# Kernel optimization log

Measured on AMD Instinct MI355X. Metric: run time of the kernel, lower is better.

## Reference

```python
import jax, jax.numpy as jnp
import numpy as np

B, N, DIN, DOUT = 8, 2048, 512, 512
EDGE_P = 0.01  # edge probability for the random binary adjacency


def setup_inputs() -> dict:
    key = jax.random.key(0)
    k1, k2, k3, k4 = jax.random.split(key, 4)
    inputs = jax.random.normal(k1, (B, N, DIN), dtype=jnp.float32)
    # binary dense adjacency (dense_to_sparse discards weights -> edges are adj != 0)
    adj = (jax.random.uniform(k2, (B, N, N)) < EDGE_P).astype(jnp.float32)
    W = jax.random.normal(k3, (DIN, DOUT), dtype=jnp.float32) / np.sqrt(DIN)
    b = jax.random.normal(k4, (DOUT,), dtype=jnp.float32) * 0.01
    return {"inputs": inputs, "adj": adj, "W": W, "b": b}


def _gcn_norm(adj):
    # binary edge mask (edge weights from dense_to_sparse are discarded)
    A = (adj != 0).astype(adj.dtype)
    # add remaining self-loops: force diagonal to 1
    eye = jnp.eye(A.shape[-1], dtype=A.dtype)
    A = jnp.maximum(A, eye)
    deg = A.sum(axis=-1)                       # [B, N]
    dinv = jnp.where(deg > 0, jax.lax.rsqrt(deg), 0.0)
    # D^-1/2 (A + I) D^-1/2
    return dinv[..., :, None] * A * dinv[..., None, :]


def reference(inputs, adj, W, b):
    norm = _gcn_norm(adj)                      # [B, N, N]
    h = jnp.einsum('bnf,fo->bno', inputs, W)   # linear (no internal bias)
    agg = jnp.einsum('bnm,bmo->bno', norm, h)  # degree-normalized aggregation
    return jnp.tanh(agg + b)
```

## Files before the change

### kernel.cpp

```cpp
#include <hip/hip_runtime.h>
#include <hip/hip_bf16.h>
#include <math.h>


#define NROWS 16384
#define NCOLS 2048
#define DF    512
#define CAP   64

typedef __attribute__((ext_vector_type(8))) short bf16x8;
typedef __attribute__((ext_vector_type(4))) float f32x4;
typedef const void __attribute__((address_space(1))) gvoid_t;
typedef void __attribute__((address_space(3))) svoid_t;

__global__ __launch_bounds__(256) void scan_wt_cvt(
    const float* __restrict__ W, __hip_bfloat16* __restrict__ WT,
    const float* __restrict__ adj, int* __restrict__ cnt,
    int* __restrict__ edges, float* __restrict__ dinv,
    const float* __restrict__ X, __hip_bfloat16* __restrict__ Xb) {
  __shared__ float t[64][65];
  const int blk = blockIdx.x;
  const int tid = threadIdx.x;
  if (blk < 64) {
    const int bx = blk & 7, by = blk >> 3;
    const int tx = tid & 63, ty = tid >> 6;
    #pragma unroll
    for (int i = 0; i < 16; ++i)
      t[ty + i * 4][tx] = W[(size_t)(by * 64 + ty + i * 4) * DF + bx * 64 + tx];
    __syncthreads();
    #pragma unroll
    for (int i = 0; i < 16; ++i)
      WT[(size_t)(bx * 64 + ty + i * 4) * DF + by * 64 + tx] =
          __float2bfloat16(t[tx][ty + i * 4]);
    return;
  }
  if (blk >= 1088) {
    const int b = blk - 1088;
    const float4* X4 = (const float4*)X;
    ushort4* O4 = (ushort4*)Xb;
    #pragma unroll
    for (int i = 0; i < 4; ++i) {
      const int idx = b * 1024 + i * 256 + tid;
      const float4 v = X4[idx];
      union { ushort4 u; __hip_bfloat16 h[4]; } p;
      p.h[0] = __float2bfloat16(v.x);
      p.h[1] = __float2bfloat16(v.y);
      p.h[2] = __float2bfloat16(v.z);
      p.h[3] = __float2bfloat16(v.w);
      O4[idx] = p.u;
    }
    return;
  }
  const int lane = tid & 63;
  const int wv = tid >> 6;
  const int rbase = (blk - 64) * 16 + wv * 4;
  float4 cur[8], nxt[8];
  {
    const float4* r4 = (const float4*)(adj + (size_t)rbase * NCOLS);
    #pragma unroll
    for (int k = 0; k < 8; ++k) cur[k] = r4[k * 64 + lane];
  }
  #pragma unroll
  for (int g = 0; g < 4; ++g) {
    const int r = rbase + g;
    if (g < 3) {
      const float4* rn = (const float4*)(adj + (size_t)(r + 1) * NCOLS);
      #pragma unroll
      for (int k = 0; k < 8; ++k) nxt[k] = rn[k * 64 + lane];
    }
    const int n = r & (NCOLS - 1);
    unsigned m = 0;
    #pragma unroll
    for (int k = 0; k < 8; ++k) {
      m |= (cur[k].x != 0.0f ? 1u : 0u) << (4 * k);
      m |= (cur[k].y != 0.0f ? 1u : 0u) << (4 * k + 1);
      m |= (cur[k].z != 0.0f ? 1u : 0u) << (4 * k + 2);
      m |= (cur[k].w != 0.0f ? 1u : 0u) << (4 * k + 3);
    }
    if (lane == ((n >> 2) & 63))
      m |= 1u << (((n >> 8) << 2) | (n & 3));
    const int c_ = __popc(m);
    int inc = c_;
    #pragma unroll
    for (int off = 1; off < 64; off <<= 1) {
      const int tv = __shfl_up(inc, off);
      if (lane >= off) inc += tv;
    }
    const int tot = __shfl(inc, 63);
    int p = inc - c_;
    unsigned mm = m;
    const size_t eb = (size_t)r * CAP;
    while (mm) {
      const int bpos = __ffs(mm) - 1;
      mm &= mm - 1;
      if (p < CAP)
        edges[eb + p] = ((bpos >> 2) << 8) + (lane << 2) + (bpos & 3);
      ++p;
    }
    if (lane == 63) {
      cnt[r] = tot < CAP ? tot : CAP;
      dinv[r] = rsqrtf((float)tot);
    }
    #pragma unroll
    for (int k = 0; k < 8; ++k) cur[k] = nxt[k];
  }
}

__global__ __launch_bounds__(256) void gemm_k(
    const __hip_bfloat16* __restrict__ A, const __hip_bfloat16* __restrict__ BT,
    __hip_bfloat16* __restrict__ H) {
  __shared__ __hip_bfloat16 As[2][128 * 32];
  __shared__ __hip_bfloat16 Bs[2][128 * 32];
  const int tid = threadIdx.x;
  const int lane = tid & 63;
  const int w = tid >> 6;
  const int id = blockIdx.x;
  const int xcd = id & 7;
  const int jj = id >> 3;
  const int bm = (xcd * 16 + (jj >> 2)) * 128;
  const int bn = (jj & 3) * 128;

  const int wm = (w >> 1) * 64;
  const int wn = (w & 1) * 64;
  const int srow = tid >> 2;
  const int scol = (tid & 3) * 8;
  const int kl = (lane >> 4) * 8;
  const int rl = lane & 15;

  f32x4 acc[4][4] = {};

  #define STAGE(k0, buf)  do {                                          \
    _Pragma("unroll")                                                   \
    for (int i = 0; i < 2; ++i) {                                       \
      const __hip_bfloat16* ga = A  + (size_t)(bm + i * 64 + srow) * DF + (k0) + scol; \
      const __hip_bfloat16* gb = BT + (size_t)(bn + i * 64 + srow) * DF + (k0) + scol; \
      char* la = (char*)&As[buf][0] + i * 4096 + w * 1024;              \
      char* lb = (char*)&Bs[buf][0] + i * 4096 + w * 1024;              \
      __builtin_amdgcn_global_load_lds((gvoid_t*)ga, (svoid_t*)la, 16, 0, 0); \
      __builtin_amdgcn_global_load_lds((gvoid_t*)gb, (svoid_t*)lb, 16, 0, 0); \
    } } while (0)

  STAGE(0, 0);
  __syncthreads();

  for (int tIt = 0; tIt < 16; ++tIt) {
    const int c_ = tIt & 1, nx = c_ ^ 1;
    if (tIt < 15) STAGE((tIt + 1) * 32, nx);
    bf16x8 af[4], bf[4];
    #pragma unroll
    for (int mi = 0; mi < 4; ++mi)
      af[mi] = *(const bf16x8*)&As[c_][(wm + mi * 16 + rl) * 32 + kl];
    #pragma unroll
    for (int ni = 0; ni < 4; ++ni)
      bf[ni] = *(const bf16x8*)&Bs[c_][(wn + ni * 16 + rl) * 32 + kl];
    #pragma unroll
    for (int mi = 0; mi < 4; ++mi)
      #pragma unroll
      for (int ni = 0; ni < 4; ++ni)
        acc[mi][ni] = __builtin_amdgcn_mfma_f32_16x16x32_bf16(af[mi], bf[ni], acc[mi][ni], 0, 0, 0);
    __syncthreads();
  }

  const int rq = (lane >> 4) * 4;
  #pragma unroll
  for (int mi = 0; mi < 4; ++mi)
    #pragma unroll
    for (int ni = 0; ni < 4; ++ni) {
      const int col = bn + wn + ni * 16 + rl;
      #pragma unroll
      for (int j = 0; j < 4; ++j) {
        const int row = bm + wm + mi * 16 + rq + j;
        H[(size_t)row * DF + col] = __float2bfloat16(acc[mi][ni][j]);
      }
    }
  #undef STAGE
}

__device__ __forceinline__ float fast_tanh(float x) {
  const float t = __expf(2.0f * x);
  return 1.0f - __fdividef(2.0f, t + 1.0f);
}

__global__ __launch_bounds__(256) void aggregate(
    const __hip_bfloat16* __restrict__ h, const int* __restrict__ cnt,
    const int* __restrict__ edges, const float* __restrict__ dinv,
    const float* __restrict__ bias, float* __restrict__ out) {
  const int lane = threadIdx.x & 63;
  const int wv = threadIdx.x >> 6;
  const int batch = blockIdx.x & 7;
  const int qb = blockIdx.x >> 3;
  const int rn = qb * 4 + wv;
  const int r = (batch << 11) + rn;
  const int c = cnt[r];
  const float* dv = dinv + (batch << 11);
  const uint4* hbase = (const uint4*)(h + (size_t)(batch << 11) * DF);
  const int* eb = edges + (size_t)r * CAP;

  float acc[8] = {0.f,0.f,0.f,0.f,0.f,0.f,0.f,0.f};
  for (int e = 0; e < c; e += 8) {
    int   mj[8];
    float wj[8];
    uint4 vj[8];
    #pragma unroll
    for (int j = 0; j < 8; ++j)
      if (e + j < c) mj[j] = eb[e + j];
    #pragma unroll
    for (int j = 0; j < 8; ++j)
      if (e + j < c) {
        wj[j] = dv[mj[j]];
        vj[j] = hbase[(size_t)mj[j] * 64 + lane];
      }
    #pragma unroll
    for (int j = 0; j < 8; ++j)
      if (e + j < c) {
        const float wt = wj[j];
        acc[0] += wt * __uint_as_float(vj[j].x << 16);
        acc[1] += wt * __uint_as_float(vj[j].x & 0xffff0000u);
        acc[2] += wt * __uint_as_float(vj[j].y << 16);
        acc[3] += wt * __uint_as_float(vj[j].y & 0xffff0000u);
        acc[4] += wt * __uint_as_float(vj[j].z << 16);
        acc[5] += wt * __uint_as_float(vj[j].z & 0xffff0000u);
        acc[6] += wt * __uint_as_float(vj[j].w << 16);
        acc[7] += wt * __uint_as_float(vj[j].w & 0xffff0000u);
      }
  }
  const float4* b4 = (const float4*)bias;
  const float4 bb0 = b4[lane * 2];
  const float4 bb1 = b4[lane * 2 + 1];
  const float dn = dv[rn];
  float4 o;
  float* op = out + (size_t)r * DF + lane * 8;
  o.x = fast_tanh(acc[0] * dn + bb0.x);
  o.y = fast_tanh(acc[1] * dn + bb0.y);
  o.z = fast_tanh(acc[2] * dn + bb0.z);
  o.w = fast_tanh(acc[3] * dn + bb0.w);
  *(float4*)op = o;
  o.x = fast_tanh(acc[4] * dn + bb1.x);
  o.y = fast_tanh(acc[5] * dn + bb1.y);
  o.z = fast_tanh(acc[6] * dn + bb1.z);
  o.w = fast_tanh(acc[7] * dn + bb1.w);
  *(float4*)(op + 4) = o;
}

extern "C" void kernel_launch(void* const* d_in, const int* in_sizes, int n_in,
                              void* d_out, int out_size, void* d_ws, size_t ws_size,
                              hipStream_t stream) {
  const float* X    = (const float*)d_in[0];
  const float* adj  = (const float*)d_in[1];
  const float* W    = (const float*)d_in[2];
  const float* bias = (const float*)d_in[3];
  float* out = (float*)d_out;

  char* ws = (char*)d_ws;
  __hip_bfloat16* h    = (__hip_bfloat16*)(ws);
  __hip_bfloat16* WT   = (__hip_bfloat16*)(ws + 16777216);
  float*          dinv = (float*)(ws + 17301504);
  int*            cnt  = (int*)  (ws + 17367040);
  int*            edges= (int*)  (ws + 17432576);
  __hip_bfloat16* Xb   = (__hip_bfloat16*)(ws + 21626880);

  scan_wt_cvt<<<3136, 256, 0, stream>>>(W, WT, adj, cnt, edges, dinv, X, Xb);
  gemm_k<<<512, 256, 0, stream>>>(Xb, WT, h);
  aggregate<<<4096, 256, 0, stream>>>(h, cnt, edges, dinv, bias, out);
}
```

Measured before the change: 72.55 us.

## Fold source-node dinv scaling into GEMM epilogue and prefetch edge indices

The GEMM epilogue now multiplies each output row of h by its dinv value before storing to bf16. This removes the per-edge dinv gather and multiply from the aggregation kernel. The aggregation loop also loads edge indices as int4 vectors and prefetches the next chunk of 8 while gathering the current one, which shortens the dependent-load chain. The cost is extra dinv reads in the GEMM epilogue, plus rounding to bf16 after the scaling rather than before it. Index slots past the edge count are read but never used, since the edge buffer is padded to CAP.

Measured after the change: 73.17 us. About the same (+0.9%).

```diff
diff --git a/kernel.cpp b/kernel.cpp
--- a/kernel.cpp
+++ b/kernel.cpp
@@ -108,7 +108,7 @@
 
 __global__ __launch_bounds__(256) void gemm_k(
     const __hip_bfloat16* __restrict__ A, const __hip_bfloat16* __restrict__ BT,
-    __hip_bfloat16* __restrict__ H) {
+    const float* __restrict__ dinv, __hip_bfloat16* __restrict__ H) {
   __shared__ __hip_bfloat16 As[2][128 * 32];
   __shared__ __hip_bfloat16 Bs[2][128 * 32];
   const int tid = threadIdx.x;
@@ -162,6 +162,12 @@
   }
 
   const int rq = (lane >> 4) * 4;
+  float dvv[4][4];
+  #pragma unroll
+  for (int mi = 0; mi < 4; ++mi)
+    #pragma unroll
+    for (int j = 0; j < 4; ++j)
+      dvv[mi][j] = dinv[bm + wm + mi * 16 + rq + j];
   #pragma unroll
   for (int mi = 0; mi < 4; ++mi)
     #pragma unroll
@@ -170,7 +176,7 @@
       #pragma unroll
       for (int j = 0; j < 4; ++j) {
         const int row = bm + wm + mi * 16 + rq + j;
-        H[(size_t)row * DF + col] = __float2bfloat16(acc[mi][ni][j]);
+        H[(size_t)row * DF + col] = __float2bfloat16(acc[mi][ni][j] * dvv[mi][j]);
       }
     }
   #undef STAGE
@@ -192,42 +198,39 @@
   const int rn = qb * 4 + wv;
   const int r = (batch << 11) + rn;
   const int c = cnt[r];
-  const float* dv = dinv + (batch << 11);
   const uint4* hbase = (const uint4*)(h + (size_t)(batch << 11) * DF);
-  const int* eb = edges + (size_t)r * CAP;
+  const int4* e4 = (const int4*)(edges + (size_t)r * CAP);
 
   float acc[8] = {0.f,0.f,0.f,0.f,0.f,0.f,0.f,0.f};
-  for (int e = 0; e < c; e += 8) {
-    int   mj[8];
-    float wj[8];
-    uint4 vj[8];
+  const int nch = (c + 7) >> 3;
+  int4 ia = e4[0], ib = e4[1];
+  for (int ch = 0; ch < nch; ++ch) {
+    int4 na, nb;
+    if (ch + 1 < nch) { na = e4[(ch + 1) * 2]; nb = e4[(ch + 1) * 2 + 1]; }
+    const int base = ch * 8;
+    const int idx[8] = {ia.x, ia.y, ia.z, ia.w, ib.x, ib.y, ib.z, ib.w};
+    uint4 v[8];
     #pragma unroll
     for (int j = 0; j < 8; ++j)
-      if (e + j < c) mj[j] = eb[e + j];
+      if (base + j < c) v[j] = hbase[(size_t)idx[j] * 64 + lane];
     #pragma unroll
     for (int j = 0; j < 8; ++j)
-      if (e + j < c) {
-        wj[j] = dv[mj[j]];
-        vj[j] = hbase[(size_t)mj[j] * 64 + lane];
+      if (base + j < c) {
+        acc[0] += __uint_as_float(v[j].x << 16);
+        acc[1] += __uint_as_float(v[j].x & 0xffff0000u);
+        acc[2] += __uint_as_float(v[j].y << 16);
+        acc[3] += __uint_as_float(v[j].y & 0xffff0000u);
+        acc[4] += __uint_as_float(v[j].z << 16);
+        acc[5] += __uint_as_float(v[j].z & 0xffff0000u);
+        acc[6] += __uint_as_float(v[j].w << 16);
+        acc[7] += __uint_as_float(v[j].w & 0xffff0000u);
       }
-    #pragma unroll
-    for (int j = 0; j < 8; ++j)
-      if (e + j < c) {
-        const float wt = wj[j];
-        acc[0] += wt * __uint_as_float(vj[j].x << 16);
-        acc[1] += wt * __uint_as_float(vj[j].x & 0xffff0000u);
-        acc[2] += wt * __uint_as_float(vj[j].y << 16);
-        acc[3] += wt * __uint_as_float(vj[j].y & 0xffff0000u);
-        acc[4] += wt * __uint_as_float(vj[j].z << 16);
-        acc[5] += wt * __uint_as_float(vj[j].z & 0xffff0000u);
-        acc[6] += wt * __uint_as_float(vj[j].w << 16);
-        acc[7] += wt * __uint_as_float(vj[j].w & 0xffff0000u);
-      }
+    ia = na; ib = nb;
   }
   const float4* b4 = (const float4*)bias;
   const float4 bb0 = b4[lane * 2];
   const float4 bb1 = b4[lane * 2 + 1];
-  const float dn = dv[rn];
+  const float dn = dinv[r];
   float4 o;
   float* op = out + (size_t)r * DF + lane * 8;
   o.x = fast_tanh(acc[0] * dn + bb0.x);
@@ -260,6 +263,6 @@
   __hip_bfloat16* Xb   = (__hip_bfloat16*)(ws + 21626880);
 
   scan_wt_cvt<<<3136, 256, 0, stream>>>(W, WT, adj, cnt, edges, dinv, X, Xb);
-  gemm_k<<<512, 256, 0, stream>>>(Xb, WT, h);
+  gemm_k<<<512, 256, 0, stream>>>(Xb, WT, dinv, h);
   aggregate<<<4096, 256, 0, stream>>>(h, cnt, edges, dinv, bias, out);
 }
```

## Fuse X bf16 conversion into GEMM and co-schedule adjacency scan with GEMM

Applied to the files above, without the earlier changes.

The separate X-to-bf16 conversion pass is removed. The GEMM now loads fp32 X rows into registers, converts them to bf16 and writes them into LDS, with the next tile's load overlapping the current tile's MFMA work. The adjacency scan blocks move into the same launch as the GEMM so the memory-bound scan can overlap the compute-bound GEMM. A small W transpose kernel stays separate. This removes one kernel launch and the Xb round trip through global memory, but the GEMM A path becomes register-staged instead of direct global-to-LDS, and GEMM blocks now share the GPU with scan blocks.

Result: slower. 76.53 us (+5.5%).

```diff
diff --git a/kernel.cpp b/kernel.cpp
--- a/kernel.cpp
+++ b/kernel.cpp
@@ -13,167 +13,170 @@
 typedef const void __attribute__((address_space(1))) gvoid_t;
 typedef void __attribute__((address_space(3))) svoid_t;
 
-__global__ __launch_bounds__(256) void scan_wt_cvt(
-    const float* __restrict__ W, __hip_bfloat16* __restrict__ WT,
-    const float* __restrict__ adj, int* __restrict__ cnt,
-    int* __restrict__ edges, float* __restrict__ dinv,
-    const float* __restrict__ X, __hip_bfloat16* __restrict__ Xb) {
+__global__ __launch_bounds__(256) void wt_kernel(
+    const float* __restrict__ W, __hip_bfloat16* __restrict__ WT) {
   __shared__ float t[64][65];
-  const int blk = blockIdx.x;
+  const int b2 = blockIdx.x;
+  const int bx = b2 & 7, by = b2 >> 3;
   const int tid = threadIdx.x;
-  if (blk < 64) {
-    const int bx = blk & 7, by = blk >> 3;
-    const int tx = tid & 63, ty = tid >> 6;
-    #pragma unroll
-    for (int i = 0; i < 16; ++i)
-      t[ty + i * 4][tx] = W[(size_t)(by * 64 + ty + i * 4) * DF + bx * 64 + tx];
-    __syncthreads();
-    #pragma unroll
-    for (int i = 0; i < 16; ++i)
-      WT[(size_t)(bx * 64 + ty + i * 4) * DF + by * 64 + tx] =
-          __float2bfloat16(t[tx][ty + i * 4]);
-    return;
-  }
-  if (blk >= 1088) {
-    const int b = blk - 1088;
-    const float4* X4 = (const float4*)X;
-    ushort4* O4 = (ushort4*)Xb;
-    #pragma unroll
-    for (int i = 0; i < 4; ++i) {
-      const int idx = b * 1024 + i * 256 + tid;
-      const float4 v = X4[idx];
-      union { ushort4 u; __hip_bfloat16 h[4]; } p;
-      p.h[0] = __float2bfloat16(v.x);
-      p.h[1] = __float2bfloat16(v.y);
-      p.h[2] = __float2bfloat16(v.z);
-      p.h[3] = __float2bfloat16(v.w);
-      O4[idx] = p.u;
-    }
-    return;
-  }
+  const int tx = tid & 63, ty = tid >> 6;
+  #pragma unroll
+  for (int i = 0; i < 16; ++i)
+    t[ty + i * 4][tx] = W[(size_t)(by * 64 + ty + i * 4) * DF + bx * 64 + tx];
+  __syncthreads();
+  #pragma unroll
+  for (int i = 0; i < 16; ++i)
+    WT[(size_t)(bx * 64 + ty + i * 4) * DF + by * 64 + tx] =
+        __float2bfloat16(t[tx][ty + i * 4]);
+}
+
+__global__ __launch_bounds__(256) void fused_sg(
+    const float* __restrict__ X, const __hip_bfloat16* __restrict__ WT,
+    const float* __restrict__ adj, __hip_bfloat16* __restrict__ H,
+    int* __restrict__ cnt, int* __restrict__ edges, float* __restrict__ dinv) {
+  __shared__ __hip_bfloat16 As[2][128 * 32];
+  __shared__ __hip_bfloat16 Bs[2][128 * 32];
+  const int id = blockIdx.x;
+  const int tid = threadIdx.x;
   const int lane = tid & 63;
   const int wv = tid >> 6;
-  const int rbase = (blk - 64) * 16 + wv * 4;
-  float4 cur[8], nxt[8];
-  {
-    const float4* r4 = (const float4*)(adj + (size_t)rbase * NCOLS);
-    #pragma unroll
-    for (int k = 0; k < 8; ++k) cur[k] = r4[k * 64 + lane];
+
+  if (id < 512) {
+    const int xcd = id & 7;
+    const int jj = id >> 3;
+    const int bm = (xcd * 16 + (jj >> 2)) * 128;
+    const int bn = (jj & 3) * 128;
+    const int w = wv;
+    const int wm = (w >> 1) * 64;
+    const int wn = (w & 1) * 64;
+    const int srow = tid >> 2;
+    const int scol = (tid & 3) * 8;
+    const int arow = tid >> 1;
+    const int akh  = (tid & 1) * 16;
+    const int kl = (lane >> 4) * 8;
+    const int rl = lane & 15;
+
+    f32x4 acc[4][4] = {};
+    float4 ar0, ar1, ar2, ar3;
+
+    #define LOAD_A(k0)  do {                                                  \
+      const float4* g_ = (const float4*)(X + (size_t)(bm + arow) * DF + (k0) + akh); \
+      ar0 = g_[0]; ar1 = g_[1]; ar2 = g_[2]; ar3 = g_[3]; } while (0)
+
+    #define STAGE_B(k0, buf)  do {                                            \
+      _Pragma("unroll")                                                       \
+      for (int i = 0; i < 2; ++i) {                                           \
+        const __hip_bfloat16* gb = WT + (size_t)(bn + i * 64 + srow) * DF + (k0) + scol; \
+        char* lb = (char*)&Bs[buf][0] + i * 4096 + w * 1024;                  \
+        __builtin_amdgcn_global_load_lds((gvoid_t*)gb, (svoid_t*)lb, 16, 0, 0); \
+      } } while (0)
+
+    #define WRITE_A(buf)  do {                                               \
+      float xs[16];                                                          \
+      *(float4*)&xs[0] = ar0; *(float4*)&xs[4] = ar1;                        \
+      *(float4*)&xs[8] = ar2; *(float4*)&xs[12] = ar3;                       \
+      union { __hip_bfloat16 hh[16]; uint4 q[2]; } pk;                       \
+      _Pragma("unroll")                                                      \
+      for (int i = 0; i < 16; ++i) pk.hh[i] = __float2bfloat16(xs[i]);       \
+      char* la = (char*)&As[buf][0] + arow * 64 + akh * 2;                   \
+      ((uint4*)la)[0] = pk.q[0];                                             \
+      ((uint4*)la)[1] = pk.q[1]; } while (0)
+
+    LOAD_A(0);
+    STAGE_B(0, 0);
+    WRITE_A(0);
+    __syncthreads();
+
+    for (int t = 0; t < 16; ++t) {
+      const int c_ = t & 1, nx = c_ ^ 1;
+      if (t < 15) {
+        LOAD_A((t + 1) * 32);
+        STAGE_B((t + 1) * 32, nx);
+      }
+      bf16x8 af[4], bf[4];
+      #pragma unroll
+      for (int mi = 0; mi < 4; ++mi)
+        af[mi] = *(const bf16x8*)&As[c_][(wm + mi * 16 + rl) * 32 + kl];
+      #pragma unroll
+      for (int ni = 0; ni < 4; ++ni)
+        bf[ni] = *(const bf16x8*)&Bs[c_][(wn + ni * 16 + rl) * 32 + kl];
+      #pragma unroll
+      for (int mi = 0; mi < 4; ++mi)
+        #pragma unroll
+        for (int ni = 0; ni < 4; ++ni)
+          acc[mi][ni] = __builtin_amdgcn_mfma_f32_16x16x32_bf16(af[mi], bf[ni], acc[mi][ni], 0, 0, 0);
+      if (t < 15) WRITE_A(nx);
+      __syncthreads();
+    }
+
+    const int rq = (lane >> 4) * 4;
+    #pragma unroll
+    for (int mi = 0; mi < 4; ++mi)
+      #pragma unroll
+      for (int ni = 0; ni < 4; ++ni) {
+        const int col = bn + wn + ni * 16 + rl;
+        #pragma unroll
+        for (int j = 0; j < 4; ++j) {
+          const int row = bm + wm + mi * 16 + rq + j;
+          H[(size_t)row * DF + col] = __float2bfloat16(acc[mi][ni][j]);
+        }
+      }
+    #undef LOAD_A
+    #undef STAGE_B
+    #undef WRITE_A
+  } else {
+    const int rbase = (id - 512) * 16 + wv * 4;
+    float4 cur[8], nxt[8];
+    {
+      const float4* r4 = (const float4*)(adj + (size_t)rbase * NCOLS);
+      #pragma unroll
+      for (int k = 0; k < 8; ++k) cur[k] = r4[k * 64 + lane];
+    }
+    #pragma unroll
+    for (int g = 0; g < 4; ++g) {
+      const int r = rbase + g;
+      if (g < 3) {
+        const float4* rn = (const float4*)(adj + (size_t)(r + 1) * NCOLS);
+        #pragma unroll
+        for (int k = 0; k < 8; ++k) nxt[k] = rn[k * 64 + lane];
+      }
+      const int n = r & (NCOLS - 1);
+      unsigned m = 0;
+      #pragma unroll
+      for (int k = 0; k < 8; ++k) {
+        m |= (cur[k].x != 0.0f ? 1u : 0u) << (4 * k);
+        m |= (cur[k].y != 0.0f ? 1u : 0u) << (4 * k + 1);
+        m |= (cur[k].z != 0.0f ? 1u : 0u) << (4 * k + 2);
+        m |= (cur[k].w != 0.0f ? 1u : 0u) << (4 * k + 3);
+      }
+      if (lane == ((n >> 2) & 63))
+        m |= 1u << (((n >> 8) << 2) | (n & 3));
+      const int c_ = __popc(m);
+      int inc = c_;
+      #pragma unroll
+      for (int off = 1; off < 64; off <<= 1) {
+        const int tv = __shfl_up(inc, off);
+        if (lane >= off) inc += tv;
+      }
+      const int tot = __shfl(inc, 63);
+      int p = inc - c_;
+      unsigned mm = m;
+      const size_t eb = (size_t)r * CAP;
+      while (mm) {
+        const int bpos = __ffs(mm) - 1;
+        mm &= mm - 1;
+        if (p < CAP)
+          edges[eb + p] = ((bpos >> 2) << 8) + (lane << 2) + (bpos & 3);
+        ++p;
+      }
+      if (lane == 63) {
+        cnt[r] = tot < CAP ? tot : CAP;
+        dinv[r] = rsqrtf((float)tot);
+      }
+      #pragma unroll
+      for (int k = 0; k < 8; ++k) cur[k] = nxt[k];
+    }
   }
-  #pragma unroll
-  for (int g = 0; g < 4; ++g) {
-    const int r = rbase + g;
-    if (g < 3) {
-      const float4* rn = (const float4*)(adj + (size_t)(r + 1) * NCOLS);
-      #pragma unroll
-      for (int k = 0; k < 8; ++k) nxt[k] = rn[k * 64 + lane];
-    }
-    const int n = r & (NCOLS - 1);
-    unsigned m = 0;
-    #pragma unroll
-    for (int k = 0; k < 8; ++k) {
-      m |= (cur[k].x != 0.0f ? 1u : 0u) << (4 * k);
-      m |= (cur[k].y != 0.0f ? 1u : 0u) << (4 * k + 1);
-      m |= (cur[k].z != 0.0f ? 1u : 0u) << (4 * k + 2);
-      m |= (cur[k].w != 0.0f ? 1u : 0u) << (4 * k + 3);
-    }
-    if (lane == ((n >> 2) & 63))
-      m |= 1u << (((n >> 8) << 2) | (n & 3));
-    const int c_ = __popc(m);
-    int inc = c_;
-    #pragma unroll
-    for (int off = 1; off < 64; off <<= 1) {
-      const int tv = __shfl_up(inc, off);
-      if (lane >= off) inc += tv;
-    }
-    const int tot = __shfl(inc, 63);
-    int p = inc - c_;
-    unsigned mm = m;
-    const size_t eb = (size_t)r * CAP;
-    while (mm) {
-      const int bpos = __ffs(mm) - 1;
-      mm &= mm - 1;
-      if (p < CAP)
-        edges[eb + p] = ((bpos >> 2) << 8) + (lane << 2) + (bpos & 3);
-      ++p;
-    }
-    if (lane == 63) {
-      cnt[r] = tot < CAP ? tot : CAP;
-      dinv[r] = rsqrtf((float)tot);
-    }
-    #pragma unroll
-    for (int k = 0; k < 8; ++k) cur[k] = nxt[k];
-  }
-}
-
-__global__ __launch_bounds__(256) void gemm_k(
-    const __hip_bfloat16* __restrict__ A, const __hip_bfloat16* __restrict__ BT,
-    __hip_bfloat16* __restrict__ H) {
-  __shared__ __hip_bfloat16 As[2][128 * 32];
-  __shared__ __hip_bfloat16 Bs[2][128 * 32];
-  const int tid = threadIdx.x;
-  const int lane = tid & 63;
-  const int w = tid >> 6;
-  const int id = blockIdx.x;
-  const int xcd = id & 7;
-  const int jj = id >> 3;
-  const int bm = (xcd * 16 + (jj >> 2)) * 128;
-  const int bn = (jj & 3) * 128;
-
-  const int wm = (w >> 1) * 64;
-  const int wn = (w & 1) * 64;
-  const int srow = tid >> 2;
-  const int scol = (tid & 3) * 8;
-  const int kl = (lane >> 4) * 8;
-  const int rl = lane & 15;
-
-  f32x4 acc[4][4] = {};
-
-  #define STAGE(k0, buf)  do {                                          \
-    _Pragma("unroll")                                                   \
-    for (int i = 0; i < 2; ++i) {                                       \
-      const __hip_bfloat16* ga = A  + (size_t)(bm + i * 64 + srow) * DF + (k0) + scol; \
-      const __hip_bfloat16* gb = BT + (size_t)(bn + i * 64 + srow) * DF + (k0) + scol; \
-      char* la = (char*)&As[buf][0] + i * 4096 + w * 1024;              \
-      char* lb = (char*)&Bs[buf][0] + i * 4096 + w * 1024;              \
-      __builtin_amdgcn_global_load_lds((gvoid_t*)ga, (svoid_t*)la, 16, 0, 0); \
-      __builtin_amdgcn_global_load_lds((gvoid_t*)gb, (svoid_t*)lb, 16, 0, 0); \
-    } } while (0)
-
-  STAGE(0, 0);
-  __syncthreads();
-
-  for (int tIt = 0; tIt < 16; ++tIt) {
-    const int c_ = tIt & 1, nx = c_ ^ 1;
-    if (tIt < 15) STAGE((tIt + 1) * 32, nx);
-    bf16x8 af[4], bf[4];
-    #pragma unroll
-    for (int mi = 0; mi < 4; ++mi)
-      af[mi] = *(const bf16x8*)&As[c_][(wm + mi * 16 + rl) * 32 + kl];
-    #pragma unroll
-    for (int ni = 0; ni < 4; ++ni)
-      bf[ni] = *(const bf16x8*)&Bs[c_][(wn + ni * 16 + rl) * 32 + kl];
-    #pragma unroll
-    for (int mi = 0; mi < 4; ++mi)
-      #pragma unroll
-      for (int ni = 0; ni < 4; ++ni)
-        acc[mi][ni] = __builtin_amdgcn_mfma_f32_16x16x32_bf16(af[mi], bf[ni], acc[mi][ni], 0, 0, 0);
-    __syncthreads();
-  }
-
-  const int rq = (lane >> 4) * 4;
-  #pragma unroll
-  for (int mi = 0; mi < 4; ++mi)
-    #pragma unroll
-    for (int ni = 0; ni < 4; ++ni) {
-      const int col = bn + wn + ni * 16 + rl;
-      #pragma unroll
-      for (int j = 0; j < 4; ++j) {
-        const int row = bm + wm + mi * 16 + rq + j;
-        H[(size_t)row * DF + col] = __float2bfloat16(acc[mi][ni][j]);
-      }
-    }
-  #undef STAGE
 }
 
 __device__ __forceinline__ float fast_tanh(float x) {
@@ -257,9 +260,8 @@
   float*          dinv = (float*)(ws + 17301504);
   int*            cnt  = (int*)  (ws + 17367040);
   int*            edges= (int*)  (ws + 17432576);
-  __hip_bfloat16* Xb   = (__hip_bfloat16*)(ws + 21626880);
-
-  scan_wt_cvt<<<3136, 256, 0, stream>>>(W, WT, adj, cnt, edges, dinv, X, Xb);
-  gemm_k<<<512, 256, 0, stream>>>(Xb, WT, h);
+
+  wt_kernel<<<64, 256, 0, stream>>>(W, WT);
+  fused_sg<<<1536, 256, 0, stream>>>(X, WT, adj, h, cnt, edges, dinv);
   aggregate<<<4096, 256, 0, stream>>>(h, cnt, edges, dinv, bias, out);
 }
```
